# Performance work log

Measured on AMD Instinct MI355X. Metric: run time of the kernel, lower is better.

## Reference

```python
import jax, jax.numpy as jnp
import numpy as np

B, N, R = 64, 2000, 64
EMBED, LABELS = 512, 20
GRAPH_DIM = 1  # feature is unsqueezed to [B, N, 1]


def setup_inputs() -> dict:
    key = jax.random.key(0)
    ks = jax.random.split(key, 10)
    s = 0.05
    return {
        "feature": jax.random.normal(ks[0], (B, N), dtype=jnp.float32),
        "init_graph": jax.random.uniform(ks[1], (N, N), dtype=jnp.float32),
        "theta_w": jax.random.normal(ks[2], (R, GRAPH_DIM), dtype=jnp.float32) * s,
        "theta_b": jax.random.normal(ks[3], (R,), dtype=jnp.float32) * s,
        "phi_w": jax.random.normal(ks[4], (R, GRAPH_DIM), dtype=jnp.float32) * s,
        "phi_b": jax.random.normal(ks[5], (R,), dtype=jnp.float32) * s,
        "fc1_w": jax.random.normal(ks[6], (EMBED, N), dtype=jnp.float32) * s,
        "fc1_b": jax.random.normal(ks[7], (EMBED,), dtype=jnp.float32) * s,
        "fc2_w": jax.random.normal(ks[8], (LABELS, EMBED), dtype=jnp.float32) * s,
        "fc2_b": jax.random.normal(ks[9], (LABELS,), dtype=jnp.float32) * s,
    }


def reference(feature, init_graph, theta_w, theta_b, phi_w, phi_b,
              fc1_w, fc1_b, fc2_w, fc2_b):
    # graph_feature: [B, N, 1]; Linear(1, R) => f * w[:, 0] + b
    theta_f = feature[..., None] * theta_w[:, 0] + theta_b  # [B, N, R]
    phi_f = feature[..., None] * phi_w[:, 0] + phi_b        # [B, N, R]
    # similarity: [B, N, N], scaled by sqrt(graph_dim)=1
    sim = jnp.einsum('bnr,bmr->bnm', theta_f, phi_f) / np.sqrt(GRAPH_DIM)
    relation_graph = jax.nn.softmax(sim, axis=2)            # [B, N, N]
    # (init_graph + relation_graph) @ graph_feature -> [B, N]
    relation_feature = jax.nn.relu(
        jnp.einsum('bnm,bm->bn', init_graph[None] + relation_graph, feature))
    mixed = relation_feature + feature                      # [B, N] (dropout is eval-mode identity)
    hidden = jnp.tanh(mixed @ fc1_w.T + fc1_b)              # [B, EMBED]
    logits = hidden @ fc2_w.T + fc2_b                       # [B, LABELS]
    return logits
```

## Files before the change

### kernel.cpp

```cpp
#include <hip/hip_runtime.h>
#include <math.h>

#define B 64
#define N 2000
#define R 64
#define EMBED 512
#define LABELS 20

#define NM 23
#define NK 22

#define KS_GF 8
#define KC_GF 256
#define KS_FC 16
#define KC_FC 128

#define SC_OFF 0
#define S_OFF 64
#define MIX_OFF 2048
#define HID_OFF (MIX_OFF + N * B)
#define PGF_OFF (HID_OFF + EMBED * B)
#define PFC_OFF (PGF_OFF + KS_GF * N * B)

__constant__ float c_invfact[NK] = {
    1.0f, 1.0f, 0.5f,
    1.6666666666666666e-01f, 4.1666666666666664e-02f, 8.3333333333333332e-03f,
    1.3888888888888889e-03f, 1.9841269841269841e-04f, 2.4801587301587302e-05f,
    2.7557319223985893e-06f, 2.7557319223985894e-07f, 2.5052108385441720e-08f,
    2.0876756987868100e-09f, 1.6059043836821616e-10f, 1.1470745597729726e-11f,
    7.6471637318198170e-13f, 4.7794773323873860e-14f, 2.8114572543455206e-15f,
    1.5619206968586225e-16f, 8.2206352466243300e-18f, 4.1103176233121650e-19f,
    1.9572941063391263e-20f,
};

__global__ __launch_bounds__(256) void prep_kernel(const float* __restrict__ f,
                                                   const float* __restrict__ tw,
                                                   const float* __restrict__ tb,
                                                   const float* __restrict__ pw,
                                                   float* __restrict__ sc,
                                                   float* __restrict__ S) {
    int bid = blockIdx.x;
    int tid = threadIdx.x;
    if (bid == B) {
        if (tid < R) {
            float a = tw[tid] * pw[tid];
            float c = tb[tid] * pw[tid];
            for (int off = 32; off; off >>= 1) {
                a += __shfl_down(a, off);
                c += __shfl_down(c, off);
            }
            if (tid == 0) { sc[0] = a; sc[1] = c; }
        }
        return;
    }
    const float* fb = f + (size_t)bid * N;
    double acc[NM];
#pragma unroll
    for (int k = 0; k < NM; ++k) acc[k] = 0.0;
    for (int m = tid; m < N; m += 256) {
        double x = (double)fb[m];
        double p = 1.0;
#pragma unroll
        for (int k = 0; k < NM; ++k) { acc[k] += p; p *= x; }
    }
    for (int off = 32; off; off >>= 1) {
#pragma unroll
        for (int k = 0; k < NM; ++k) acc[k] += __shfl_down(acc[k], off);
    }
    __shared__ double sred[4][NM];
    int w = tid >> 6, lane = tid & 63;
    if (lane == 0) {
#pragma unroll
        for (int k = 0; k < NM; ++k) sred[w][k] = acc[k];
    }
    __syncthreads();
    if (tid < NM) {
        double s = sred[0][tid] + sred[1][tid] + sred[2][tid] + sred[3][tid];
        S[tid * 64 + bid] = (float)s;
    }
}

__global__ __launch_bounds__(512) void gf_partial(const float* __restrict__ G,
                                                  const float* __restrict__ f,
                                                  float* __restrict__ P) {
    extern __shared__ float lds[];
    float* Gs = lds;
    float* fs = lds + 64 * KC_GF;
    int tid = threadIdx.x;
    int lane = tid & 63, w = tid >> 6;
    int nt = blockIdx.x & 31;
    int ks = blockIdx.x >> 5;
    int n0 = nt * 64, k0 = ks * KC_GF;

#pragma unroll
    for (int j = 0; j < 8; ++j) {
        int flat = tid * 4 + j * 2048;
        int r = flat >> 8, c = flat & 255;
        int n = n0 + r; if (n > N - 1) n = N - 1;
        int cc = c; if (k0 + c + 3 >= N) cc = N - 4 - k0;
        float4 g = *(const float4*)(G + (size_t)n * N + (k0 + cc));
        *(float4*)(Gs + r * KC_GF + c) = g;
    }
#pragma unroll
    for (int j = 0; j < 8; ++j) {
        int b = (tid >> 6) + j * 8;
        int c = (tid & 63) * 4;
        int kc = k0 + c;
        float4 v = make_float4(0.f, 0.f, 0.f, 0.f);
        if (kc + 3 < N) {
            v = *(const float4*)(f + (size_t)b * N + kc);
        } else {
            const float* fb = f + (size_t)b * N;
            if (kc < N) v.x = fb[kc];
            if (kc + 1 < N) v.y = fb[kc + 1];
            if (kc + 2 < N) v.z = fb[kc + 2];
        }
        float* p = fs + c * 64 + (b ^ (lane & 31));
        p[0] = v.x; p[64] = v.y; p[128] = v.z; p[192] = v.w;
    }
    __syncthreads();

    float acc[8];
#pragma unroll
    for (int r = 0; r < 8; ++r) acc[r] = 0.f;
    int nrow = w * 8;
    for (int i = 0; i < KC_GF / 4; ++i) {
        const float* fp = fs + i * 256 + (lane ^ (i & 31));
        float f0 = fp[0], f1 = fp[64], f2 = fp[128], f3 = fp[192];
#pragma unroll
        for (int r = 0; r < 8; ++r) {
            const float4 g = *(const float4*)(Gs + (nrow + r) * KC_GF + 4 * i);
            acc[r] = fmaf(g.x, f0, acc[r]);
            acc[r] = fmaf(g.y, f1, acc[r]);
            acc[r] = fmaf(g.z, f2, acc[r]);
            acc[r] = fmaf(g.w, f3, acc[r]);
        }
    }
    size_t base = ((size_t)ks * N + n0 + nrow) * 64 + lane;
#pragma unroll
    for (int r = 0; r < 8; ++r) {
        if (n0 + nrow + r < N) P[base + (size_t)r * 64] = acc[r];
    }
}

__global__ __launch_bounds__(256) void reduce_gf(const float* __restrict__ P,
                                                 const float* __restrict__ f,
                                                 const float* __restrict__ sc,
                                                 const float* __restrict__ S,
                                                 float* __restrict__ mixT) {
    int flat = blockIdx.x * 256 + threadIdx.x;
    int n = flat >> 6, b = flat & 63;
    float s = 0.f;
#pragma unroll
    for (int k = 0; k < KS_GF; ++k) s += P[(size_t)k * N * 64 + flat];
    float fn = f[(size_t)b * N + n];
    float A = sc[0], C2 = sc[1];
    float t = fmaf(A, fn, C2);
    float Z = 0.f, Wv = 0.f, tp = 1.f;
#pragma unroll
    for (int k = 0; k < NK; ++k) {
        float c = tp * c_invfact[k];
        Z = fmaf(c, S[k * 64 + b], Z);
        Wv = fmaf(c, S[(k + 1) * 64 + b], Wv);
        tp *= t;
    }
    float r = fmaxf(s + Wv / Z, 0.f);
    mixT[flat] = r + fn;
}

__global__ __launch_bounds__(256) void fc1_partial(const float* __restrict__ w1,
                                                   const float* __restrict__ mixT,
                                                   float* __restrict__ P) {
    __shared__ float Ws[32 * KC_FC];
    __shared__ float ms[KC_FC * 65];
    int tid = threadIdx.x;
    int lane = tid & 63, w = tid >> 6;
    int et = blockIdx.x & 15;
    int ks = blockIdx.x >> 4;
    int e0 = et * 32, k0 = ks * KC_FC;

#pragma unroll
    for (int j = 0; j < 4; ++j) {
        int flat = tid * 4 + j * 1024;
        int r = flat >> 7, c = flat & 127;
        int cc = c; if (k0 + c + 3 >= N) cc = N - 4 - k0;
        float4 g = *(const float4*)(w1 + (size_t)(e0 + r) * N + (k0 + cc));
        *(float4*)(Ws + r * KC_FC + c) = g;
    }
#pragma unroll
    for (int j = 0; j < 8; ++j) {
        int flat = tid * 4 + j * 1024;
        int k = flat >> 6, b4 = flat & 63;
        float4 v = make_float4(0.f, 0.f, 0.f, 0.f);
        if (k0 + k < N) v = *(const float4*)(mixT + (size_t)(k0 + k) * 64 + b4);
        float* p = ms + k * 65 + b4;
        p[0] = v.x; p[1] = v.y; p[2] = v.z; p[3] = v.w;
    }
    __syncthreads();

    float acc[8];
#pragma unroll
    for (int r = 0; r < 8; ++r) acc[r] = 0.f;
    int erow = w * 8;
    for (int i = 0; i < KC_FC / 4; ++i) {
        const float* fp = ms + (4 * i) * 65 + lane;
        float f0 = fp[0], f1 = fp[65], f2 = fp[130], f3 = fp[195];
#pragma unroll
        for (int r = 0; r < 8; ++r) {
            const float4 g = *(const float4*)(Ws + (erow + r) * KC_FC + 4 * i);
            acc[r] = fmaf(g.x, f0, acc[r]);
            acc[r] = fmaf(g.y, f1, acc[r]);
            acc[r] = fmaf(g.z, f2, acc[r]);
            acc[r] = fmaf(g.w, f3, acc[r]);
        }
    }
    size_t base = ((size_t)ks * EMBED + e0 + erow) * 64 + lane;
#pragma unroll
    for (int r = 0; r < 8; ++r) P[base + (size_t)r * 64] = acc[r];
}

__global__ __launch_bounds__(256) void reduce_fc1(const float* __restrict__ P,
                                                  const float* __restrict__ b1,
                                                  float* __restrict__ hidden) {
    int flat = blockIdx.x * 256 + threadIdx.x;
    int e = flat >> 6;
    float s = 0.f;
#pragma unroll
    for (int k = 0; k < KS_FC; ++k) s += P[(size_t)k * EMBED * 64 + flat];
    hidden[flat] = tanhf(s + b1[e]);
}

__global__ __launch_bounds__(256) void fc2_kernel(const float* __restrict__ hidden,
                                                  const float* __restrict__ w2,
                                                  const float* __restrict__ b2,
                                                  float* __restrict__ out) {
    int l = blockIdx.x;
    int tid = threadIdx.x;
    int lane = tid & 63;
    int w = tid >> 6;
    const float4* W = (const float4*)(w2 + (size_t)l * EMBED) + w * 32;
    const float* h = hidden + (size_t)(w * 128) * B + lane;
    float a0 = 0.f, a1 = 0.f, a2 = 0.f, a3 = 0.f;
#pragma unroll 4
    for (int i = 0; i < 32; ++i) {
        float4 g = W[i];
        a0 = fmaf(g.x, h[(4 * i + 0) * B], a0);
        a1 = fmaf(g.y, h[(4 * i + 1) * B], a1);
        a2 = fmaf(g.z, h[(4 * i + 2) * B], a2);
        a3 = fmaf(g.w, h[(4 * i + 3) * B], a3);
    }
    __shared__ float part[4][64];
    part[w][lane] = (a0 + a1) + (a2 + a3);
    __syncthreads();
    if (w == 0) {
        out[(size_t)lane * LABELS + l] =
            part[0][lane] + part[1][lane] + part[2][lane] + part[3][lane] + b2[l];
    }
}

extern "C" void kernel_launch(void* const* d_in, const int* in_sizes, int n_in,
                              void* d_out, int out_size, void* d_ws, size_t ws_size,
                              hipStream_t stream) {
    const float* feature = (const float*)d_in[0];
    const float* init_graph = (const float*)d_in[1];
    const float* theta_w = (const float*)d_in[2];
    const float* theta_b = (const float*)d_in[3];
    const float* phi_w = (const float*)d_in[4];
    const float* fc1_w = (const float*)d_in[6];
    const float* fc1_b = (const float*)d_in[7];
    const float* fc2_w = (const float*)d_in[8];
    const float* fc2_b = (const float*)d_in[9];
    float* out = (float*)d_out;

    float* ws = (float*)d_ws;
    float* sc = ws + SC_OFF;
    float* S = ws + S_OFF;
    float* mixT = ws + MIX_OFF;
    float* hidden = ws + HID_OFF;
    float* Pgf = ws + PGF_OFF;
    float* Pfc = ws + PFC_OFF;

    hipLaunchKernelGGL(prep_kernel, dim3(B + 1), dim3(256), 0, stream,
                       feature, theta_w, theta_b, phi_w, sc, S);
    hipLaunchKernelGGL(gf_partial, dim3(32 * KS_GF), dim3(512),
                       (64 * KC_GF + KC_GF * 64) * sizeof(float), stream,
                       init_graph, feature, Pgf);
    hipLaunchKernelGGL(reduce_gf, dim3(N * B / 256), dim3(256), 0, stream,
                       Pgf, feature, sc, S, mixT);
    hipLaunchKernelGGL(fc1_partial, dim3(16 * KS_FC), dim3(256), 0, stream,
                       fc1_w, mixT, Pfc);
    hipLaunchKernelGGL(reduce_fc1, dim3(EMBED * B / 256), dim3(256), 0, stream,
                       Pfc, fc1_b, hidden);
    hipLaunchKernelGGL(fc2_kernel, dim3(LABELS), dim3(256), 0, stream,
                       hidden, fc2_w, fc2_b, out);
}
```

Baseline: 129.3 us.

## Replace LDS-tiled GEMMs with register-resident split-K kernel and pre-transposed features

Adds a transpose of the feature matrix into a [N,64] layout inside the prep kernel. Both the graph GEMM and fc1 now use one templated split-K kernel that keeps an 80-long column of X in registers per lane and streams weight rows straight from global memory, with no LDS staging or barrier. The finer split (25 K-slices) raises block count but grows the partial-sum buffers and the reduce traffic. Register pressure from the 80-float array and uniform broadcast loads of A rows may limit occupancy.

```diff
diff --git a/kernel.cpp b/kernel.cpp
--- a/kernel.cpp
+++ b/kernel.cpp
@@ -10,17 +10,18 @@
 #define NM 23
 #define NK 22
 
-#define KS_GF 8
-#define KC_GF 256
-#define KS_FC 16
-#define KC_FC 128
+#define KS 25
+#define KC 80
+#define NT_GF 32
+#define NT_FC 8
 
 #define SC_OFF 0
 #define S_OFF 64
-#define MIX_OFF 2048
+#define FT_OFF 2048
+#define MIX_OFF (FT_OFF + N * B)
 #define HID_OFF (MIX_OFF + N * B)
 #define PGF_OFF (HID_OFF + EMBED * B)
-#define PFC_OFF (PGF_OFF + KS_GF * N * B)
+#define PFC_OFF (PGF_OFF + KS * N * B)
 
 __constant__ float c_invfact[NK] = {
     1.0f, 1.0f, 0.5f,
@@ -33,15 +34,28 @@
     1.9572941063391263e-20f,
 };
 
-__global__ __launch_bounds__(256) void prep_kernel(const float* __restrict__ f,
-                                                   const float* __restrict__ tw,
-                                                   const float* __restrict__ tb,
-                                                   const float* __restrict__ pw,
-                                                   float* __restrict__ sc,
-                                                   float* __restrict__ S) {
+__global__ __launch_bounds__(256) void prep_fused(const float* __restrict__ f,
+                                                  const float* __restrict__ tw,
+                                                  const float* __restrict__ tb,
+                                                  const float* __restrict__ pw,
+                                                  float* __restrict__ sc,
+                                                  float* __restrict__ S,
+                                                  float* __restrict__ fT) {
+    __shared__ float tile[64][65];
+    __shared__ double sred[4][NM];
     int bid = blockIdx.x;
     int tid = threadIdx.x;
-    if (bid == B) {
+    if (bid >= 65) {
+        int m0 = (bid - 65) * 64;
+        int lane = tid & 63, w = tid >> 6;
+        for (int bb = w; bb < 64; bb += 4)
+            tile[lane][bb] = (m0 + lane < N) ? f[(size_t)bb * N + m0 + lane] : 0.f;
+        __syncthreads();
+        for (int mm = w; mm < 64; mm += 4)
+            if (m0 + mm < N) fT[(size_t)(m0 + mm) * 64 + lane] = tile[mm][lane];
+        return;
+    }
+    if (bid == 64) {
         if (tid < R) {
             float a = tw[tid] * pw[tid];
             float c = tb[tid] * pw[tid];
@@ -67,7 +81,6 @@
 #pragma unroll
         for (int k = 0; k < NM; ++k) acc[k] += __shfl_down(acc[k], off);
     }
-    __shared__ double sred[4][NM];
     int w = tid >> 6, lane = tid & 63;
     if (lane == 0) {
 #pragma unroll
@@ -80,80 +93,59 @@
     }
 }
 
-__global__ __launch_bounds__(512) void gf_partial(const float* __restrict__ G,
-                                                  const float* __restrict__ f,
-                                                  float* __restrict__ P) {
-    extern __shared__ float lds[];
-    float* Gs = lds;
-    float* fs = lds + 64 * KC_GF;
+template <int M>
+__global__ __launch_bounds__(512) void gemm_part(const float* __restrict__ A,
+                                                 const float* __restrict__ X,
+                                                 float* __restrict__ P) {
     int tid = threadIdx.x;
-    int lane = tid & 63, w = tid >> 6;
-    int nt = blockIdx.x & 31;
-    int ks = blockIdx.x >> 5;
-    int n0 = nt * 64, k0 = ks * KC_GF;
-
-#pragma unroll
-    for (int j = 0; j < 8; ++j) {
-        int flat = tid * 4 + j * 2048;
-        int r = flat >> 8, c = flat & 255;
-        int n = n0 + r; if (n > N - 1) n = N - 1;
-        int cc = c; if (k0 + c + 3 >= N) cc = N - 4 - k0;
-        float4 g = *(const float4*)(G + (size_t)n * N + (k0 + cc));
-        *(float4*)(Gs + r * KC_GF + c) = g;
-    }
-#pragma unroll
-    for (int j = 0; j < 8; ++j) {
-        int b = (tid >> 6) + j * 8;
-        int c = (tid & 63) * 4;
-        int kc = k0 + c;
-        float4 v = make_float4(0.f, 0.f, 0.f, 0.f);
-        if (kc + 3 < N) {
-            v = *(const float4*)(f + (size_t)b * N + kc);
-        } else {
-            const float* fb = f + (size_t)b * N;
-            if (kc < N) v.x = fb[kc];
-            if (kc + 1 < N) v.y = fb[kc + 1];
-            if (kc + 2 < N) v.z = fb[kc + 2];
+    int lane = tid & 63;
+    int w = __builtin_amdgcn_readfirstlane(tid >> 6);
+    int ks = blockIdx.x % KS;
+    int nt = blockIdx.x / KS;
+    int k0 = ks * KC;
+    int row0 = nt * 64 + w * 8;
+
+    float vf[KC];
+#pragma unroll
+    for (int j = 0; j < KC; ++j) vf[j] = X[(size_t)(k0 + j) * 64 + lane];
+
+    int rowc[8];
+#pragma unroll
+    for (int r = 0; r < 8; ++r) rowc[r] = (row0 + r < M) ? (row0 + r) : (M - 1);
+
+    float acc[8];
+#pragma unroll
+    for (int r = 0; r < 8; ++r) acc[r] = 0.f;
+
+#pragma unroll
+    for (int j4 = 0; j4 < KC / 4; ++j4) {
+#pragma unroll
+        for (int r = 0; r < 8; ++r) {
+            const float4 g = *(const float4*)(A + (size_t)rowc[r] * N + k0 + 4 * j4);
+            acc[r] = fmaf(g.x, vf[4 * j4 + 0], acc[r]);
+            acc[r] = fmaf(g.y, vf[4 * j4 + 1], acc[r]);
+            acc[r] = fmaf(g.z, vf[4 * j4 + 2], acc[r]);
+            acc[r] = fmaf(g.w, vf[4 * j4 + 3], acc[r]);
         }
-        float* p = fs + c * 64 + (b ^ (lane & 31));
-        p[0] = v.x; p[64] = v.y; p[128] = v.z; p[192] = v.w;
-    }
-    __syncthreads();
-
-    float acc[8];
-#pragma unroll
-    for (int r = 0; r < 8; ++r) acc[r] = 0.f;
-    int nrow = w * 8;
-    for (int i = 0; i < KC_GF / 4; ++i) {
-        const float* fp = fs + i * 256 + (lane ^ (i & 31));
-        float f0 = fp[0], f1 = fp[64], f2 = fp[128], f3 = fp[192];
-#pragma unroll
-        for (int r = 0; r < 8; ++r) {
-            const float4 g = *(const float4*)(Gs + (nrow + r) * KC_GF + 4 * i);
-            acc[r] = fmaf(g.x, f0, acc[r]);
-            acc[r] = fmaf(g.y, f1, acc[r]);
-            acc[r] = fmaf(g.z, f2, acc[r]);
-            acc[r] = fmaf(g.w, f3, acc[r]);
-        }
-    }
-    size_t base = ((size_t)ks * N + n0 + nrow) * 64 + lane;
+    }
 #pragma unroll
     for (int r = 0; r < 8; ++r) {
-        if (n0 + nrow + r < N) P[base + (size_t)r * 64] = acc[r];
+        int row = row0 + r;
+        if (row < M) P[((size_t)ks * M + row) * 64 + lane] = acc[r];
     }
 }
 
 __global__ __launch_bounds__(256) void reduce_gf(const float* __restrict__ P,
-                                                 const float* __restrict__ f,
+                                                 const float* __restrict__ fT,
                                                  const float* __restrict__ sc,
                                                  const float* __restrict__ S,
                                                  float* __restrict__ mixT) {
     int flat = blockIdx.x * 256 + threadIdx.x;
-    int n = flat >> 6, b = flat & 63;
+    int b = flat & 63;
     float s = 0.f;
 #pragma unroll
-    for (int k = 0; k < KS_GF; ++k) s += P[(size_t)k * N * 64 + flat];
-    float fn = f[(size_t)b * N + n];
+    for (int k = 0; k < KS; ++k) s += P[(size_t)k * N * 64 + flat];
+    float fn = fT[flat];
     float A = sc[0], C2 = sc[1];
     float t = fmaf(A, fn, C2);
     float Z = 0.f, Wv = 0.f, tp = 1.f;
@@ -166,57 +158,6 @@
     }
     float r = fmaxf(s + Wv / Z, 0.f);
     mixT[flat] = r + fn;
-}
-
-__global__ __launch_bounds__(256) void fc1_partial(const float* __restrict__ w1,
-                                                   const float* __restrict__ mixT,
-                                                   float* __restrict__ P) {
-    __shared__ float Ws[32 * KC_FC];
-    __shared__ float ms[KC_FC * 65];
-    int tid = threadIdx.x;
-    int lane = tid & 63, w = tid >> 6;
-    int et = blockIdx.x & 15;
-    int ks = blockIdx.x >> 4;
-    int e0 = et * 32, k0 = ks * KC_FC;
-
-#pragma unroll
-    for (int j = 0; j < 4; ++j) {
-        int flat = tid * 4 + j * 1024;
-        int r = flat >> 7, c = flat & 127;
-        int cc = c; if (k0 + c + 3 >= N) cc = N - 4 - k0;
-        float4 g = *(const float4*)(w1 + (size_t)(e0 + r) * N + (k0 + cc));
-        *(float4*)(Ws + r * KC_FC + c) = g;
-    }
-#pragma unroll
-    for (int j = 0; j < 8; ++j) {
-        int flat = tid * 4 + j * 1024;
-        int k = flat >> 6, b4 = flat & 63;
-        float4 v = make_float4(0.f, 0.f, 0.f, 0.f);
-        if (k0 + k < N) v = *(const float4*)(mixT + (size_t)(k0 + k) * 64 + b4);
-        float* p = ms + k * 65 + b4;
-        p[0] = v.x; p[1] = v.y; p[2] = v.z; p[3] = v.w;
-    }
-    __syncthreads();
-
-    float acc[8];
-#pragma unroll
-    for (int r = 0; r < 8; ++r) acc[r] = 0.f;
-    int erow = w * 8;
-    for (int i = 0; i < KC_FC / 4; ++i) {
-        const float* fp = ms + (4 * i) * 65 + lane;
-        float f0 = fp[0], f1 = fp[65], f2 = fp[130], f3 = fp[195];
-#pragma unroll
-        for (int r = 0; r < 8; ++r) {
-            const float4 g = *(const float4*)(Ws + (erow + r) * KC_FC + 4 * i);
-            acc[r] = fmaf(g.x, f0, acc[r]);
-            acc[r] = fmaf(g.y, f1, acc[r]);
-            acc[r] = fmaf(g.z, f2, acc[r]);
-            acc[r] = fmaf(g.w, f3, acc[r]);
-        }
-    }
-    size_t base = ((size_t)ks * EMBED + e0 + erow) * 64 + lane;
-#pragma unroll
-    for (int r = 0; r < 8; ++r) P[base + (size_t)r * 64] = acc[r];
 }
 
 __global__ __launch_bounds__(256) void reduce_fc1(const float* __restrict__ P,
@@ -226,7 +167,7 @@
     int e = flat >> 6;
     float s = 0.f;
 #pragma unroll
-    for (int k = 0; k < KS_FC; ++k) s += P[(size_t)k * EMBED * 64 + flat];
+    for (int k = 0; k < KS; ++k) s += P[(size_t)k * EMBED * 64 + flat];
     hidden[flat] = tanhf(s + b1[e]);
 }
 
@@ -275,19 +216,19 @@
     float* ws = (float*)d_ws;
     float* sc = ws + SC_OFF;
     float* S = ws + S_OFF;
+    float* fT = ws + FT_OFF;
     float* mixT = ws + MIX_OFF;
     float* hidden = ws + HID_OFF;
     float* Pgf = ws + PGF_OFF;
     float* Pfc = ws + PFC_OFF;
 
-    hipLaunchKernelGGL(prep_kernel, dim3(B + 1), dim3(256), 0, stream,
-                       feature, theta_w, theta_b, phi_w, sc, S);
-    hipLaunchKernelGGL(gf_partial, dim3(32 * KS_GF), dim3(512),
-                       (64 * KC_GF + KC_GF * 64) * sizeof(float), stream,
-                       init_graph, feature, Pgf);
+    hipLaunchKernelGGL(prep_fused, dim3(65 + (N + 63) / 64), dim3(256), 0, stream,
+                       feature, theta_w, theta_b, phi_w, sc, S, fT);
+    hipLaunchKernelGGL((gemm_part<N>), dim3(NT_GF * KS), dim3(512), 0, stream,
+                       init_graph, fT, Pgf);
     hipLaunchKernelGGL(reduce_gf, dim3(N * B / 256), dim3(256), 0, stream,
-                       Pgf, feature, sc, S, mixT);
-    hipLaunchKernelGGL(fc1_partial, dim3(16 * KS_FC), dim3(256), 0, stream,
+                       Pgf, fT, sc, S, mixT);
+    hipLaunchKernelGGL((gemm_part<EMBED>), dim3(NT_FC * KS), dim3(512), 0, stream,
                        fc1_w, mixT, Pfc);
     hipLaunchKernelGGL(reduce_fc1, dim3(EMBED * B / 256), dim3(256), 0, stream,
                        Pfc, fc1_b, hidden);
```

New measurement: 125.1 us. -3.3%, faster.
